# Optimization experiments

Hardware: AMD Instinct MI355X
Metric: run time of the kernel (lower is better)

Reference implementation:

```python
import jax, jax.numpy as jnp
import numpy as np

N_GRAPHS = 1024
N_NODES = 65536
N_EDGES = 262144
D = 256          # node/edge/global feature dim
D_IN = 3 * D     # concat of edge_agg, node_agg, globals
D_HID = 512
D_OUT = 256


def setup_inputs() -> dict:
    key = jax.random.key(0)
    ks = jax.random.split(key, 9)
    nodes = jax.random.normal(ks[0], (N_NODES, D), dtype=jnp.float32)
    edges = jax.random.normal(ks[1], (N_EDGES, D), dtype=jnp.float32)
    globals_ = jax.random.normal(ks[2], (N_GRAPHS, D), dtype=jnp.float32)
    node_graph_ids = jnp.sort(jax.random.randint(ks[3], (N_NODES,), 0, N_GRAPHS, dtype=jnp.int32))
    edge_graph_ids = jnp.sort(jax.random.randint(ks[4], (N_EDGES,), 0, N_GRAPHS, dtype=jnp.int32))
    W1 = jax.random.normal(ks[5], (D_IN, D_HID), dtype=jnp.float32) * (1.0 / np.sqrt(D_IN))
    b1 = jnp.zeros((D_HID,), dtype=jnp.float32)
    W2 = jax.random.normal(ks[6], (D_HID, D_OUT), dtype=jnp.float32) * (1.0 / np.sqrt(D_HID))
    b2 = jnp.zeros((D_OUT,), dtype=jnp.float32)
    return {"nodes": nodes, "edges": edges, "globals_": globals_,
            "node_graph_ids": node_graph_ids, "edge_graph_ids": edge_graph_ids,
            "W1": W1, "b1": b1, "W2": W2, "b2": b2}


def reference(nodes, edges, globals_, node_graph_ids, edge_graph_ids, W1, b1, W2, b2):
    G = globals_.shape[0]
    # EdgesToGlobalsAggregator / NodesToGlobalsAggregator: unsorted segment sum per graph
    edge_agg = jax.ops.segment_sum(edges, edge_graph_ids, num_segments=G)  # [G, D]
    node_agg = jax.ops.segment_sum(nodes, node_graph_ids, num_segments=G)  # [G, D]
    collected = jnp.concatenate([edge_agg, node_agg, globals_], axis=-1)   # [G, 3D]
    # global_model: 2-layer MLP with ReLU
    h = jax.nn.relu(collected @ W1 + b1)
    updated_globals = h @ W2 + b2
    return updated_globals
```

## Files before the change

kernel.cpp:

```cpp
#include <hip/hip_runtime.h>

#define G      1024
#define NNODES 65536
#define NEDGES 262144
#define D      256
#define DIN    768
#define DHID   512
#define DOUT   256

__device__ __forceinline__ int lower_bound(const int* __restrict__ a, int n, int key) {
    int lo = 0, hi = n;
    while (lo < hi) {
        const int mid = (lo + hi) >> 1;
        if (a[mid] < key) lo = mid + 1; else hi = mid;
    }
    return lo;
}

__global__ __launch_bounds__(256) void fused_agg(
        const float4* __restrict__ nodes,
        const float4* __restrict__ edges,
        const float4* __restrict__ globals_,
        const int* __restrict__ nids,
        const int* __restrict__ eids,
        float* __restrict__ collected) {
    const int g    = blockIdx.x;
    const int lane = threadIdx.x & 63;
    const int wave = threadIdx.x >> 6;

    const int es = lower_bound(eids, NEDGES, g);
    const int ee = lower_bound(eids, NEDGES, g + 1);
    const int ns = lower_bound(nids, NNODES, g);
    const int ne = lower_bound(nids, NNODES, g + 1);

    float4 acc_e = {0.f, 0.f, 0.f, 0.f};
    {
        int r = es + wave;
        for (; r + 28 < ee; r += 32) {
            const float4 v0 = edges[(size_t)(r +  0) * (D / 4) + lane];
            const float4 v1 = edges[(size_t)(r +  4) * (D / 4) + lane];
            const float4 v2 = edges[(size_t)(r +  8) * (D / 4) + lane];
            const float4 v3 = edges[(size_t)(r + 12) * (D / 4) + lane];
            const float4 v4 = edges[(size_t)(r + 16) * (D / 4) + lane];
            const float4 v5 = edges[(size_t)(r + 20) * (D / 4) + lane];
            const float4 v6 = edges[(size_t)(r + 24) * (D / 4) + lane];
            const float4 v7 = edges[(size_t)(r + 28) * (D / 4) + lane];
            acc_e.x += ((v0.x + v1.x) + (v2.x + v3.x)) + ((v4.x + v5.x) + (v6.x + v7.x));
            acc_e.y += ((v0.y + v1.y) + (v2.y + v3.y)) + ((v4.y + v5.y) + (v6.y + v7.y));
            acc_e.z += ((v0.z + v1.z) + (v2.z + v3.z)) + ((v4.z + v5.z) + (v6.z + v7.z));
            acc_e.w += ((v0.w + v1.w) + (v2.w + v3.w)) + ((v4.w + v5.w) + (v6.w + v7.w));
        }
        for (; r < ee; r += 4) {
            const float4 v = edges[(size_t)r * (D / 4) + lane];
            acc_e.x += v.x; acc_e.y += v.y; acc_e.z += v.z; acc_e.w += v.w;
        }
    }

    float4 acc_n = {0.f, 0.f, 0.f, 0.f};
    {
        int r = ns + wave;
        for (; r + 28 < ne; r += 32) {
            const float4 v0 = nodes[(size_t)(r +  0) * (D / 4) + lane];
            const float4 v1 = nodes[(size_t)(r +  4) * (D / 4) + lane];
            const float4 v2 = nodes[(size_t)(r +  8) * (D / 4) + lane];
            const float4 v3 = nodes[(size_t)(r + 12) * (D / 4) + lane];
            const float4 v4 = nodes[(size_t)(r + 16) * (D / 4) + lane];
            const float4 v5 = nodes[(size_t)(r + 20) * (D / 4) + lane];
            const float4 v6 = nodes[(size_t)(r + 24) * (D / 4) + lane];
            const float4 v7 = nodes[(size_t)(r + 28) * (D / 4) + lane];
            acc_n.x += ((v0.x + v1.x) + (v2.x + v3.x)) + ((v4.x + v5.x) + (v6.x + v7.x));
            acc_n.y += ((v0.y + v1.y) + (v2.y + v3.y)) + ((v4.y + v5.y) + (v6.y + v7.y));
            acc_n.z += ((v0.z + v1.z) + (v2.z + v3.z)) + ((v4.z + v5.z) + (v6.z + v7.z));
            acc_n.w += ((v0.w + v1.w) + (v2.w + v3.w)) + ((v4.w + v5.w) + (v6.w + v7.w));
        }
        for (; r < ne; r += 4) {
            const float4 v = nodes[(size_t)r * (D / 4) + lane];
            acc_n.x += v.x; acc_n.y += v.y; acc_n.z += v.z; acc_n.w += v.w;
        }
    }

    __shared__ __align__(16) float se[4][D];
    __shared__ __align__(16) float sn[4][D];
    *(float4*)&se[wave][lane * 4] = acc_e;
    *(float4*)&sn[wave][lane * 4] = acc_n;
    __syncthreads();

    const int t = threadIdx.x;
    const float ev = (se[0][t] + se[1][t]) + (se[2][t] + se[3][t]);
    const float nv = (sn[0][t] + sn[1][t]) + (sn[2][t] + sn[3][t]);
    float* row = collected + (size_t)g * DIN;
    row[t]         = ev;
    row[D + t]     = nv;
    row[2 * D + t] = ((const float*)globals_)[(size_t)g * D + t];
}

template <int TM, int TN, int TK>
__global__ __launch_bounds__(256) void gemm_bias_act(
        const float* __restrict__ A, const float* __restrict__ B,
        const float* __restrict__ bias, float* __restrict__ C,
        int M, int N, int K, int relu) {
    __shared__ float At[2][TK][TM + 2];
    __shared__ __align__(16) float Bs[2][TK][TN];

    const int tid = threadIdx.x;
    const int tx = tid & 15;
    const int ty = tid >> 4;
    const int m0 = blockIdx.y * TM;
    const int n0 = blockIdx.x * TN;

    const int ar = tid >> 3;
    const int ac = (tid & 7) * 4;
    const int br = tid >> 3;
    const int bc = (tid & 7) * 8;

    const float* Aptr = A + (size_t)(m0 + ar) * K + ac;
    const float* Bptr = B + (size_t)br * N + n0 + bc;

    {
        const float4 a4  = *(const float4*)Aptr;
        const float4 b40 = *(const float4*)Bptr;
        const float4 b41 = *(const float4*)(Bptr + 4);
        At[0][ac + 0][ar] = a4.x; At[0][ac + 1][ar] = a4.y;
        At[0][ac + 2][ar] = a4.z; At[0][ac + 3][ar] = a4.w;
        *(float4*)&Bs[0][br][bc]     = b40;
        *(float4*)&Bs[0][br][bc + 4] = b41;
    }
    __syncthreads();

    float4 acc0 = {0.f, 0.f, 0.f, 0.f};
    float4 acc1 = {0.f, 0.f, 0.f, 0.f};
    int buf = 0;

    for (int kt = 0; kt < K; kt += TK) {
        const bool has_next = (kt + TK) < K;
        float4 na, nb0, nb1;
        if (has_next) {
            na  = *(const float4*)(Aptr + kt + TK);
            nb0 = *(const float4*)(Bptr + (size_t)(kt + TK) * N);
            nb1 = *(const float4*)(Bptr + (size_t)(kt + TK) * N + 4);
        }
#pragma unroll
        for (int k = 0; k < TK; ++k) {
            const float2 a2 = *(const float2*)&At[buf][k][ty * 2];
            const float4 bv = *(const float4*)&Bs[buf][k][tx * 4];
            acc0.x += a2.x * bv.x; acc0.y += a2.x * bv.y;
            acc0.z += a2.x * bv.z; acc0.w += a2.x * bv.w;
            acc1.x += a2.y * bv.x; acc1.y += a2.y * bv.y;
            acc1.z += a2.y * bv.z; acc1.w += a2.y * bv.w;
        }
        if (has_next) {
            const int nb = buf ^ 1;
            At[nb][ac + 0][ar] = na.x; At[nb][ac + 1][ar] = na.y;
            At[nb][ac + 2][ar] = na.z; At[nb][ac + 3][ar] = na.w;
            *(float4*)&Bs[nb][br][bc]     = nb0;
            *(float4*)&Bs[nb][br][bc + 4] = nb1;
            __syncthreads();
            buf = nb;
        }
    }

    const int col = n0 + tx * 4;
    const int row = m0 + ty * 2;
    const float4 bv = *(const float4*)&bias[col];
    float4 o0, o1;
    o0.x = acc0.x + bv.x; o0.y = acc0.y + bv.y; o0.z = acc0.z + bv.z; o0.w = acc0.w + bv.w;
    o1.x = acc1.x + bv.x; o1.y = acc1.y + bv.y; o1.z = acc1.z + bv.z; o1.w = acc1.w + bv.w;
    if (relu) {
        o0.x = fmaxf(o0.x, 0.f); o0.y = fmaxf(o0.y, 0.f);
        o0.z = fmaxf(o0.z, 0.f); o0.w = fmaxf(o0.w, 0.f);
        o1.x = fmaxf(o1.x, 0.f); o1.y = fmaxf(o1.y, 0.f);
        o1.z = fmaxf(o1.z, 0.f); o1.w = fmaxf(o1.w, 0.f);
    }
    *(float4*)&C[(size_t)row * N + col] = o0;
    *(float4*)&C[(size_t)(row + 1) * N + col] = o1;
}

extern "C" void kernel_launch(void* const* d_in, const int* in_sizes, int n_in,
                              void* d_out, int out_size, void* d_ws, size_t ws_size,
                              hipStream_t stream) {
    const float* nodes    = (const float*)d_in[0];
    const float* edges    = (const float*)d_in[1];
    const float* globals_ = (const float*)d_in[2];
    const int*   nids     = (const int*)d_in[3];
    const int*   eids     = (const int*)d_in[4];
    const float* W1       = (const float*)d_in[5];
    const float* b1       = (const float*)d_in[6];
    const float* W2       = (const float*)d_in[7];
    const float* b2       = (const float*)d_in[8];
    float* out = (float*)d_out;

    float* collected = (float*)d_ws;
    float* h         = collected + (size_t)G * DIN;

    fused_agg<<<G, 256, 0, stream>>>(
        (const float4*)nodes, (const float4*)edges, (const float4*)globals_,
        nids, eids, collected);

    gemm_bias_act<32, 64, 32><<<dim3(DHID / 64, G / 32), 256, 0, stream>>>(
        collected, W1, b1, h, G, DHID, DIN, 1);

    gemm_bias_act<32, 64, 32><<<dim3(DOUT / 64, G / 32), 256, 0, stream>>>(
        h, W2, b2, out, G, DOUT, DHID, 0);
}
```

Measured before the change: 465.2 us.

## Fuse aggregation and both MLP GEMMs into one persistent kernel with group counters

Replaces three kernel launches with a single 512-block kernel. Each block aggregates two graphs, then computes GEMM1 tiles and GEMM2 tiles, waiting on per-row-group atomic counters instead of kernel boundaries. The aim is to remove launch gaps and tail idle time between stages, and to let GEMM work start as soon as its 32 input rows are ready. The cost is a memset launch for the counters and spin-waits that depend on all 512 blocks being resident at once (launch_bounds 256,2), which deadlocks if they are not co-resident.

```diff
diff --git a/kernel.cpp b/kernel.cpp
--- a/kernel.cpp
+++ b/kernel.cpp
@@ -8,6 +8,12 @@
 #define DHID   512
 #define DOUT   256
 
+#define NBLK   512
+#define GRP    32
+#define NGRP   (G / GRP)
+#define G1_BLOCKS (NGRP * (DHID / 64))
+#define G2_BLOCKS (NGRP * (DOUT / 64))
+
 __device__ __forceinline__ int lower_bound(const int* __restrict__ a, int n, int key) {
     int lo = 0, hi = n;
     while (lo < hi) {
@@ -17,14 +23,13 @@
     return lo;
 }
 
-__global__ __launch_bounds__(256) void fused_agg(
-        const float4* __restrict__ nodes,
-        const float4* __restrict__ edges,
-        const float4* __restrict__ globals_,
-        const int* __restrict__ nids,
-        const int* __restrict__ eids,
-        float* __restrict__ collected) {
-    const int g    = blockIdx.x;
+struct LdsRed { float se[4][D]; float sn[4][D]; };
+struct LdsGemm { float At[2][32][34]; float Bs[2][32][64]; };
+
+__device__ __forceinline__ void aggregate_one(
+        int g, const float4* __restrict__ nodes, const float4* __restrict__ edges,
+        const float4* __restrict__ globals_, const int* __restrict__ nids,
+        const int* __restrict__ eids, float* __restrict__ collected, LdsRed* red) {
     const int lane = threadIdx.x & 63;
     const int wave = threadIdx.x >> 6;
 
@@ -55,7 +60,6 @@
             acc_e.x += v.x; acc_e.y += v.y; acc_e.z += v.z; acc_e.w += v.w;
         }
     }
-
     float4 acc_n = {0.f, 0.f, 0.f, 0.f};
     {
         int r = ns + wave;
@@ -79,35 +83,27 @@
         }
     }
 
-    __shared__ __align__(16) float se[4][D];
-    __shared__ __align__(16) float sn[4][D];
-    *(float4*)&se[wave][lane * 4] = acc_e;
-    *(float4*)&sn[wave][lane * 4] = acc_n;
+    *(float4*)&red->se[wave][lane * 4] = acc_e;
+    *(float4*)&red->sn[wave][lane * 4] = acc_n;
     __syncthreads();
 
     const int t = threadIdx.x;
-    const float ev = (se[0][t] + se[1][t]) + (se[2][t] + se[3][t]);
-    const float nv = (sn[0][t] + sn[1][t]) + (sn[2][t] + sn[3][t]);
+    const float ev = (red->se[0][t] + red->se[1][t]) + (red->se[2][t] + red->se[3][t]);
+    const float nv = (red->sn[0][t] + red->sn[1][t]) + (red->sn[2][t] + red->sn[3][t]);
     float* row = collected + (size_t)g * DIN;
     row[t]         = ev;
     row[D + t]     = nv;
     row[2 * D + t] = ((const float*)globals_)[(size_t)g * D + t];
 }
 
-template <int TM, int TN, int TK>
-__global__ __launch_bounds__(256) void gemm_bias_act(
+__device__ __forceinline__ void gemm_tile(
         const float* __restrict__ A, const float* __restrict__ B,
         const float* __restrict__ bias, float* __restrict__ C,
-        int M, int N, int K, int relu) {
-    __shared__ float At[2][TK][TM + 2];
-    __shared__ __align__(16) float Bs[2][TK][TN];
-
+        const int N, const int K, const int relu, const int m0, const int n0,
+        LdsGemm* gg) {
     const int tid = threadIdx.x;
     const int tx = tid & 15;
     const int ty = tid >> 4;
-    const int m0 = blockIdx.y * TM;
-    const int n0 = blockIdx.x * TN;
-
     const int ar = tid >> 3;
     const int ac = (tid & 7) * 4;
     const int br = tid >> 3;
@@ -120,10 +116,10 @@
         const float4 a4  = *(const float4*)Aptr;
         const float4 b40 = *(const float4*)Bptr;
         const float4 b41 = *(const float4*)(Bptr + 4);
-        At[0][ac + 0][ar] = a4.x; At[0][ac + 1][ar] = a4.y;
-        At[0][ac + 2][ar] = a4.z; At[0][ac + 3][ar] = a4.w;
-        *(float4*)&Bs[0][br][bc]     = b40;
-        *(float4*)&Bs[0][br][bc + 4] = b41;
+        gg->At[0][ac + 0][ar] = a4.x; gg->At[0][ac + 1][ar] = a4.y;
+        gg->At[0][ac + 2][ar] = a4.z; gg->At[0][ac + 3][ar] = a4.w;
+        *(float4*)&gg->Bs[0][br][bc]     = b40;
+        *(float4*)&gg->Bs[0][br][bc + 4] = b41;
     }
     __syncthreads();
 
@@ -131,18 +127,18 @@
     float4 acc1 = {0.f, 0.f, 0.f, 0.f};
     int buf = 0;
 
-    for (int kt = 0; kt < K; kt += TK) {
-        const bool has_next = (kt + TK) < K;
+    for (int kt = 0; kt < K; kt += 32) {
+        const bool has_next = (kt + 32) < K;
         float4 na, nb0, nb1;
         if (has_next) {
-            na  = *(const float4*)(Aptr + kt + TK);
-            nb0 = *(const float4*)(Bptr + (size_t)(kt + TK) * N);
-            nb1 = *(const float4*)(Bptr + (size_t)(kt + TK) * N + 4);
+            na  = *(const float4*)(Aptr + kt + 32);
+            nb0 = *(const float4*)(Bptr + (size_t)(kt + 32) * N);
+            nb1 = *(const float4*)(Bptr + (size_t)(kt + 32) * N + 4);
         }
 #pragma unroll
-        for (int k = 0; k < TK; ++k) {
-            const float2 a2 = *(const float2*)&At[buf][k][ty * 2];
-            const float4 bv = *(const float4*)&Bs[buf][k][tx * 4];
+        for (int k = 0; k < 32; ++k) {
+            const float2 a2 = *(const float2*)&gg->At[buf][k][ty * 2];
+            const float4 bv = *(const float4*)&gg->Bs[buf][k][tx * 4];
             acc0.x += a2.x * bv.x; acc0.y += a2.x * bv.y;
             acc0.z += a2.x * bv.z; acc0.w += a2.x * bv.w;
             acc1.x += a2.y * bv.x; acc1.y += a2.y * bv.y;
@@ -150,10 +146,10 @@
         }
         if (has_next) {
             const int nb = buf ^ 1;
-            At[nb][ac + 0][ar] = na.x; At[nb][ac + 1][ar] = na.y;
-            At[nb][ac + 2][ar] = na.z; At[nb][ac + 3][ar] = na.w;
-            *(float4*)&Bs[nb][br][bc]     = nb0;
-            *(float4*)&Bs[nb][br][bc + 4] = nb1;
+            gg->At[nb][ac + 0][ar] = na.x; gg->At[nb][ac + 1][ar] = na.y;
+            gg->At[nb][ac + 2][ar] = na.z; gg->At[nb][ac + 3][ar] = na.w;
+            *(float4*)&gg->Bs[nb][br][bc]     = nb0;
+            *(float4*)&gg->Bs[nb][br][bc + 4] = nb1;
             __syncthreads();
             buf = nb;
         }
@@ -175,30 +171,82 @@
     *(float4*)&C[(size_t)(row + 1) * N + col] = o1;
 }
 
+__device__ __forceinline__ void signal_group(unsigned int* c) {
+    __threadfence();
+    __syncthreads();
+    if (threadIdx.x == 0)
+        __hip_atomic_fetch_add(c, 1u, __ATOMIC_RELEASE, __HIP_MEMORY_SCOPE_AGENT);
+}
+
+__device__ __forceinline__ void wait_group(unsigned int* c, unsigned int target) {
+    if (threadIdx.x == 0)
+        while (__hip_atomic_load(c, __ATOMIC_RELAXED, __HIP_MEMORY_SCOPE_AGENT) < target)
+            __builtin_amdgcn_s_sleep(2);
+    __syncthreads();
+    __builtin_amdgcn_fence(__ATOMIC_ACQUIRE, "agent");
+}
+
+__global__ __launch_bounds__(256, 2) void fused_all(
+        const float4* __restrict__ nodes,
+        const float4* __restrict__ edges,
+        const float4* __restrict__ globals_,
+        const int* __restrict__ nids,
+        const int* __restrict__ eids,
+        const float* __restrict__ W1, const float* __restrict__ b1,
+        const float* __restrict__ W2, const float* __restrict__ b2,
+        float* __restrict__ collected, float* __restrict__ h,
+        float* __restrict__ out,
+        unsigned int* __restrict__ cnt1, unsigned int* __restrict__ cnt2) {
+    __shared__ __align__(16) union { LdsRed red; LdsGemm gg; } lds;
+
+    const int b = blockIdx.x;
+
+    aggregate_one(b, nodes, edges, globals_, nids, eids, collected, &lds.red);
+    signal_group(&cnt1[b >> 5]);
+    __syncthreads();
+    aggregate_one(b + NBLK, nodes, edges, globals_, nids, eids, collected, &lds.red);
+    signal_group(&cnt1[(b + NBLK) >> 5]);
+
+    if (b >= G1_BLOCKS) return;
+
+    {
+        const int mg = b >> 3, ng = b & 7;
+        wait_group(&cnt1[mg], GRP);
+        gemm_tile(collected, W1, b1, h, DHID, DIN, 1, mg * 32, ng * 64, &lds.gg);
+    }
+    signal_group(&cnt2[b >> 3]);
+
+    if (b >= G2_BLOCKS) return;
+
+    {
+        const int mg = b >> 2, ng = b & 3;
+        wait_group(&cnt2[mg], 8u);
+        gemm_tile(h, W2, b2, out, DOUT, DHID, 0, mg * 32, ng * 64, &lds.gg);
+    }
+}
+
 extern "C" void kernel_launch(void* const* d_in, const int* in_sizes, int n_in,
                               void* d_out, int out_size, void* d_ws, size_t ws_size,
                               hipStream_t stream) {
-    const float* nodes    = (const float*)d_in[0];
-    const float* edges    = (const float*)d_in[1];
-    const float* globals_ = (const float*)d_in[2];
-    const int*   nids     = (const int*)d_in[3];
-    const int*   eids     = (const int*)d_in[4];
-    const float* W1       = (const float*)d_in[5];
-    const float* b1       = (const float*)d_in[6];
-    const float* W2       = (const float*)d_in[7];
-    const float* b2       = (const float*)d_in[8];
+    const float4* nodes    = (const float4*)d_in[0];
+    const float4* edges    = (const float4*)d_in[1];
+    const float4* globals_ = (const float4*)d_in[2];
+    const int*    nids     = (const int*)d_in[3];
+    const int*    eids     = (const int*)d_in[4];
+    const float*  W1       = (const float*)d_in[5];
+    const float*  b1       = (const float*)d_in[6];
+    const float*  W2       = (const float*)d_in[7];
+    const float*  b2       = (const float*)d_in[8];
     float* out = (float*)d_out;
 
     float* collected = (float*)d_ws;
     float* h         = collected + (size_t)G * DIN;
-
-    fused_agg<<<G, 256, 0, stream>>>(
-        (const float4*)nodes, (const float4*)edges, (const float4*)globals_,
-        nids, eids, collected);
-
-    gemm_bias_act<32, 64, 32><<<dim3(DHID / 64, G / 32), 256, 0, stream>>>(
-        collected, W1, b1, h, G, DHID, DIN, 1);
-
-    gemm_bias_act<32, 64, 32><<<dim3(DOUT / 64, G / 32), 256, 0, stream>>>(
-        h, W2, b2, out, G, DOUT, DHID, 0);
-}
+    unsigned int* cnt1 = (unsigned int*)((char*)d_ws + (size_t)(G * DIN + G * DHID) * sizeof(float));
+    unsigned int* cnt2 = cnt1 + NGRP;
+
+    hipMemsetAsync(cnt1, 0, 2 * NGRP * sizeof(unsigned int), stream);
+
+    fused_all<<<NBLK, 256, 0, stream>>>(
+        nodes, edges, globals_, nids, eids, W1, b1, W2, b2,
+        collected, h, out, cnt1, cnt2);
+}
```

New measurement: 679.1 us. 1.46x slower.

## Precompute segment offsets in a separate kernel and widen aggregation blocks to 8 waves

Applied to the files above, without the earlier changes.

Moves the four per-block binary searches into a small build_offsets kernel that writes CSR-style offset arrays to the workspace, so each aggregation block just reads two pairs of ints. The aggregation kernel now runs 512 threads (8 waves) per graph, each wave striding by 8 rows with an 8-deep unroll, which puts more loads in flight per segment. Final reduction is split so half the threads sum edges and half sum nodes. This costs an extra kernel launch, and with about 256 edge rows per graph the unrolled loop runs only a few iterations per wave, so more of the work falls into the remainder loop.

```diff
diff --git a/kernel.cpp b/kernel.cpp
--- a/kernel.cpp
+++ b/kernel.cpp
@@ -17,81 +17,94 @@
     return lo;
 }
 
-__global__ __launch_bounds__(256) void fused_agg(
+__global__ __launch_bounds__(256) void build_offsets(
+        const int* __restrict__ eids, const int* __restrict__ nids,
+        int* __restrict__ eoff, int* __restrict__ noff) {
+    const int t = blockIdx.x * 256 + threadIdx.x;
+    if (t <= G)              eoff[t]         = lower_bound(eids, NEDGES, t);
+    else if (t <= 2 * G + 1) noff[t - G - 1] = lower_bound(nids, NNODES, t - G - 1);
+}
+
+__global__ __launch_bounds__(512, 8) void fused_agg(
         const float4* __restrict__ nodes,
         const float4* __restrict__ edges,
         const float4* __restrict__ globals_,
-        const int* __restrict__ nids,
-        const int* __restrict__ eids,
+        const int* __restrict__ eoff,
+        const int* __restrict__ noff,
         float* __restrict__ collected) {
+    __shared__ __align__(16) float se[8][D];
+    __shared__ __align__(16) float sn[8][D];
+
     const int g    = blockIdx.x;
     const int lane = threadIdx.x & 63;
     const int wave = threadIdx.x >> 6;
 
-    const int es = lower_bound(eids, NEDGES, g);
-    const int ee = lower_bound(eids, NEDGES, g + 1);
-    const int ns = lower_bound(nids, NNODES, g);
-    const int ne = lower_bound(nids, NNODES, g + 1);
-
-    float4 acc_e = {0.f, 0.f, 0.f, 0.f};
+    const int es = eoff[g], ee = eoff[g + 1];
+    const int ns = noff[g], ne = noff[g + 1];
+
     {
+        float4 acc = {0.f, 0.f, 0.f, 0.f};
         int r = es + wave;
-        for (; r + 28 < ee; r += 32) {
-            const float4 v0 = edges[(size_t)(r +  0) * (D / 4) + lane];
-            const float4 v1 = edges[(size_t)(r +  4) * (D / 4) + lane];
-            const float4 v2 = edges[(size_t)(r +  8) * (D / 4) + lane];
-            const float4 v3 = edges[(size_t)(r + 12) * (D / 4) + lane];
-            const float4 v4 = edges[(size_t)(r + 16) * (D / 4) + lane];
-            const float4 v5 = edges[(size_t)(r + 20) * (D / 4) + lane];
-            const float4 v6 = edges[(size_t)(r + 24) * (D / 4) + lane];
-            const float4 v7 = edges[(size_t)(r + 28) * (D / 4) + lane];
-            acc_e.x += ((v0.x + v1.x) + (v2.x + v3.x)) + ((v4.x + v5.x) + (v6.x + v7.x));
-            acc_e.y += ((v0.y + v1.y) + (v2.y + v3.y)) + ((v4.y + v5.y) + (v6.y + v7.y));
-            acc_e.z += ((v0.z + v1.z) + (v2.z + v3.z)) + ((v4.z + v5.z) + (v6.z + v7.z));
-            acc_e.w += ((v0.w + v1.w) + (v2.w + v3.w)) + ((v4.w + v5.w) + (v6.w + v7.w));
-        }
-        for (; r < ee; r += 4) {
+        for (; r + 56 < ee; r += 64) {
+            const float4* p = edges + (size_t)r * (D / 4) + lane;
+            const float4 v0 = p[0 * 8 * (D / 4)];
+            const float4 v1 = p[1 * 8 * (D / 4)];
+            const float4 v2 = p[2 * 8 * (D / 4)];
+            const float4 v3 = p[3 * 8 * (D / 4)];
+            const float4 v4 = p[4 * 8 * (D / 4)];
+            const float4 v5 = p[5 * 8 * (D / 4)];
+            const float4 v6 = p[6 * 8 * (D / 4)];
+            const float4 v7 = p[7 * 8 * (D / 4)];
+            acc.x += ((v0.x + v1.x) + (v2.x + v3.x)) + ((v4.x + v5.x) + (v6.x + v7.x));
+            acc.y += ((v0.y + v1.y) + (v2.y + v3.y)) + ((v4.y + v5.y) + (v6.y + v7.y));
+            acc.z += ((v0.z + v1.z) + (v2.z + v3.z)) + ((v4.z + v5.z) + (v6.z + v7.z));
+            acc.w += ((v0.w + v1.w) + (v2.w + v3.w)) + ((v4.w + v5.w) + (v6.w + v7.w));
+        }
+        for (; r < ee; r += 8) {
             const float4 v = edges[(size_t)r * (D / 4) + lane];
-            acc_e.x += v.x; acc_e.y += v.y; acc_e.z += v.z; acc_e.w += v.w;
-        }
-    }
-
-    float4 acc_n = {0.f, 0.f, 0.f, 0.f};
+            acc.x += v.x; acc.y += v.y; acc.z += v.z; acc.w += v.w;
+        }
+        *(float4*)&se[wave][lane * 4] = acc;
+    }
     {
+        float4 acc = {0.f, 0.f, 0.f, 0.f};
         int r = ns + wave;
-        for (; r + 28 < ne; r += 32) {
-            const float4 v0 = nodes[(size_t)(r +  0) * (D / 4) + lane];
-            const float4 v1 = nodes[(size_t)(r +  4) * (D / 4) + lane];
-            const float4 v2 = nodes[(size_t)(r +  8) * (D / 4) + lane];
-            const float4 v3 = nodes[(size_t)(r + 12) * (D / 4) + lane];
-            const float4 v4 = nodes[(size_t)(r + 16) * (D / 4) + lane];
-            const float4 v5 = nodes[(size_t)(r + 20) * (D / 4) + lane];
-            const float4 v6 = nodes[(size_t)(r + 24) * (D / 4) + lane];
-            const float4 v7 = nodes[(size_t)(r + 28) * (D / 4) + lane];
-            acc_n.x += ((v0.x + v1.x) + (v2.x + v3.x)) + ((v4.x + v5.x) + (v6.x + v7.x));
-            acc_n.y += ((v0.y + v1.y) + (v2.y + v3.y)) + ((v4.y + v5.y) + (v6.y + v7.y));
-            acc_n.z += ((v0.z + v1.z) + (v2.z + v3.z)) + ((v4.z + v5.z) + (v6.z + v7.z));
-            acc_n.w += ((v0.w + v1.w) + (v2.w + v3.w)) + ((v4.w + v5.w) + (v6.w + v7.w));
-        }
-        for (; r < ne; r += 4) {
+        for (; r + 56 < ne; r += 64) {
+            const float4* p = nodes + (size_t)r * (D / 4) + lane;
+            const float4 v0 = p[0 * 8 * (D / 4)];
+            const float4 v1 = p[1 * 8 * (D / 4)];
+            const float4 v2 = p[2 * 8 * (D / 4)];
+            const float4 v3 = p[3 * 8 * (D / 4)];
+            const float4 v4 = p[4 * 8 * (D / 4)];
+            const float4 v5 = p[5 * 8 * (D / 4)];
+            const float4 v6 = p[6 * 8 * (D / 4)];
+            const float4 v7 = p[7 * 8 * (D / 4)];
+            acc.x += ((v0.x + v1.x) + (v2.x + v3.x)) + ((v4.x + v5.x) + (v6.x + v7.x));
+            acc.y += ((v0.y + v1.y) + (v2.y + v3.y)) + ((v4.y + v5.y) + (v6.y + v7.y));
+            acc.z += ((v0.z + v1.z) + (v2.z + v3.z)) + ((v4.z + v5.z) + (v6.z + v7.z));
+            acc.w += ((v0.w + v1.w) + (v2.w + v3.w)) + ((v4.w + v5.w) + (v6.w + v7.w));
+        }
+        for (; r < ne; r += 8) {
             const float4 v = nodes[(size_t)r * (D / 4) + lane];
-            acc_n.x += v.x; acc_n.y += v.y; acc_n.z += v.z; acc_n.w += v.w;
-        }
-    }
-
-    __shared__ __align__(16) float se[4][D];
-    __shared__ __align__(16) float sn[4][D];
-    *(float4*)&se[wave][lane * 4] = acc_e;
-    *(float4*)&sn[wave][lane * 4] = acc_n;
+            acc.x += v.x; acc.y += v.y; acc.z += v.z; acc.w += v.w;
+        }
+        *(float4*)&sn[wave][lane * 4] = acc;
+    }
     __syncthreads();
 
-    const int t = threadIdx.x;
-    const float ev = (se[0][t] + se[1][t]) + (se[2][t] + se[3][t]);
-    const float nv = (sn[0][t] + sn[1][t]) + (sn[2][t] + sn[3][t]);
     float* row = collected + (size_t)g * DIN;
-    row[t]         = ev;
-    row[D + t]     = nv;
-    row[2 * D + t] = ((const float*)globals_)[(size_t)g * D + t];
+    if (threadIdx.x < D) {
+        const int t = threadIdx.x;
+        const float ev = ((se[0][t] + se[1][t]) + (se[2][t] + se[3][t]))
+                       + ((se[4][t] + se[5][t]) + (se[6][t] + se[7][t]));
+        row[t]         = ev;
+        row[2 * D + t] = ((const float*)globals_)[(size_t)g * D + t];
+    } else {
+        const int t = threadIdx.x - D;
+        const float nv = ((sn[0][t] + sn[1][t]) + (sn[2][t] + sn[3][t]))
+                       + ((sn[4][t] + sn[5][t]) + (sn[6][t] + sn[7][t]));
+        row[D + t] = nv;
+    }
 }
 
 template <int TM, int TN, int TK>
@@ -191,10 +204,14 @@
 
     float* collected = (float*)d_ws;
     float* h         = collected + (size_t)G * DIN;
-
-    fused_agg<<<G, 256, 0, stream>>>(
+    int*   eoff      = (int*)(h + (size_t)G * DHID);
+    int*   noff      = eoff + (G + 1);
+
+    build_offsets<<<(2 * (G + 1) + 255) / 256, 256, 0, stream>>>(eids, nids, eoff, noff);
+
+    fused_agg<<<G, 512, 0, stream>>>(
         (const float4*)nodes, (const float4*)edges, (const float4*)globals_,
-        nids, eids, collected);
+        eoff, noff, collected);
 
     gemm_bias_act<32, 64, 32><<<dim3(DHID / 64, G / 32), 256, 0, stream>>>(
         collected, W1, b1, h, G, DHID, DIN, 1);
```

After: 464.0 us. Within noise of the previous version (-0.3%).

## Split segment sums into fixed row chunks with atomic flushes; read globals directly in GEMM

Applied to the files above, without the earlier changes.

Segment aggregation no longer runs one block per graph with binary-search bounds. Each wave now sums a fixed contiguous chunk of edge and node rows, tracking graph-id boundaries and flushing partial sums with atomicAdd into a zeroed buffer. This balances work across waves regardless of graph size and software-pipelines the loads. The first GEMM reads the globals input directly through a split-A loader instead of copying it into the concatenated buffer. The cost is an extra memset, float atomics that make summation order nondeterministic, and chunk sizes hardcoded to the exact row counts.

```diff
diff --git a/kernel.cpp b/kernel.cpp
--- a/kernel.cpp
+++ b/kernel.cpp
@@ -7,117 +7,122 @@
 #define DIN    768
 #define DHID   512
 #define DOUT   256
-
-__device__ __forceinline__ int lower_bound(const int* __restrict__ a, int n, int key) {
-    int lo = 0, hi = n;
-    while (lo < hi) {
-        const int mid = (lo + hi) >> 1;
-        if (a[mid] < key) lo = mid + 1; else hi = mid;
-    }
-    return lo;
-}
-
-__global__ __launch_bounds__(256) void fused_agg(
+#define CW     512
+
+#define AGG_BLOCKS 1024
+#define EROWS      64
+#define NROWS      16
+
+__device__ __forceinline__ void flush_acc(float* __restrict__ dst, int cur, int col,
+                                          float4& acc) {
+    float* p = dst + (size_t)cur * CW + col;
+    atomicAdd(p + 0, acc.x); atomicAdd(p + 1, acc.y);
+    atomicAdd(p + 2, acc.z); atomicAdd(p + 3, acc.w);
+    acc.x = acc.y = acc.z = acc.w = 0.f;
+}
+
+__device__ __forceinline__ void row_step(int id, const float4 v, int& cur, float4& acc,
+                                         float* __restrict__ dst, int col) {
+    if (id != cur) { flush_acc(dst, cur, col, acc); cur = id; }
+    acc.x += v.x; acc.y += v.y; acc.z += v.z; acc.w += v.w;
+}
+
+__device__ __forceinline__ void load_group(const float4* __restrict__ src,
+                                           const int* __restrict__ ids, int r, int lane,
+                                           float4 v[8], int4& i0, int4& i1) {
+    const float4* p = src + (size_t)r * (D / 4) + lane;
+#pragma unroll
+    for (int j = 0; j < 8; ++j) v[j] = p[j * (D / 4)];
+    i0 = *(const int4*)&ids[r];
+    i1 = *(const int4*)&ids[r + 4];
+}
+
+__device__ __forceinline__ void proc_group(const float4 v[8], int4 i0, int4 i1,
+                                           int& cur, float4& acc,
+                                           float* __restrict__ dst, int col) {
+    if (i0.x == cur && i1.w == cur) {
+        acc.x += ((v[0].x + v[1].x) + (v[2].x + v[3].x)) + ((v[4].x + v[5].x) + (v[6].x + v[7].x));
+        acc.y += ((v[0].y + v[1].y) + (v[2].y + v[3].y)) + ((v[4].y + v[5].y) + (v[6].y + v[7].y));
+        acc.z += ((v[0].z + v[1].z) + (v[2].z + v[3].z)) + ((v[4].z + v[5].z) + (v[6].z + v[7].z));
+        acc.w += ((v[0].w + v[1].w) + (v[2].w + v[3].w)) + ((v[4].w + v[5].w) + (v[6].w + v[7].w));
+    } else {
+        row_step(i0.x, v[0], cur, acc, dst, col);
+        row_step(i0.y, v[1], cur, acc, dst, col);
+        row_step(i0.z, v[2], cur, acc, dst, col);
+        row_step(i0.w, v[3], cur, acc, dst, col);
+        row_step(i1.x, v[4], cur, acc, dst, col);
+        row_step(i1.y, v[5], cur, acc, dst, col);
+        row_step(i1.z, v[6], cur, acc, dst, col);
+        row_step(i1.w, v[7], cur, acc, dst, col);
+    }
+}
+
+__device__ __forceinline__ void seg_sum_pipelined(
+        const float4* __restrict__ src, const int* __restrict__ ids,
+        float* __restrict__ dst, int col, int r, int ngroups, int lane) {
+    float4 va[8], vb[8];
+    int4 ia0, ia1, ib0, ib1;
+    float4 acc = {0.f, 0.f, 0.f, 0.f};
+    int cur = ids[r];
+
+    load_group(src, ids, r, lane, va, ia0, ia1);
+    for (int gpair = 0; gpair < ngroups / 2 - 1; ++gpair) {
+        load_group(src, ids, r + 8, lane, vb, ib0, ib1);
+        proc_group(va, ia0, ia1, cur, acc, dst, col);
+        r += 8;
+        load_group(src, ids, r + 8, lane, va, ia0, ia1);
+        proc_group(vb, ib0, ib1, cur, acc, dst, col);
+        r += 8;
+    }
+    load_group(src, ids, r + 8, lane, vb, ib0, ib1);
+    proc_group(va, ia0, ia1, cur, acc, dst, col);
+    proc_group(vb, ib0, ib1, cur, acc, dst, col);
+    flush_acc(dst, cur, col, acc);
+}
+
+__global__ __launch_bounds__(256, 4) void fused_agg(
         const float4* __restrict__ nodes,
         const float4* __restrict__ edges,
-        const float4* __restrict__ globals_,
         const int* __restrict__ nids,
         const int* __restrict__ eids,
         float* __restrict__ collected) {
-    const int g    = blockIdx.x;
     const int lane = threadIdx.x & 63;
     const int wave = threadIdx.x >> 6;
-
-    const int es = lower_bound(eids, NEDGES, g);
-    const int ee = lower_bound(eids, NEDGES, g + 1);
-    const int ns = lower_bound(nids, NNODES, g);
-    const int ne = lower_bound(nids, NNODES, g + 1);
-
-    float4 acc_e = {0.f, 0.f, 0.f, 0.f};
-    {
-        int r = es + wave;
-        for (; r + 28 < ee; r += 32) {
-            const float4 v0 = edges[(size_t)(r +  0) * (D / 4) + lane];
-            const float4 v1 = edges[(size_t)(r +  4) * (D / 4) + lane];
-            const float4 v2 = edges[(size_t)(r +  8) * (D / 4) + lane];
-            const float4 v3 = edges[(size_t)(r + 12) * (D / 4) + lane];
-            const float4 v4 = edges[(size_t)(r + 16) * (D / 4) + lane];
-            const float4 v5 = edges[(size_t)(r + 20) * (D / 4) + lane];
-            const float4 v6 = edges[(size_t)(r + 24) * (D / 4) + lane];
-            const float4 v7 = edges[(size_t)(r + 28) * (D / 4) + lane];
-            acc_e.x += ((v0.x + v1.x) + (v2.x + v3.x)) + ((v4.x + v5.x) + (v6.x + v7.x));
-            acc_e.y += ((v0.y + v1.y) + (v2.y + v3.y)) + ((v4.y + v5.y) + (v6.y + v7.y));
-            acc_e.z += ((v0.z + v1.z) + (v2.z + v3.z)) + ((v4.z + v5.z) + (v6.z + v7.z));
-            acc_e.w += ((v0.w + v1.w) + (v2.w + v3.w)) + ((v4.w + v5.w) + (v6.w + v7.w));
-        }
-        for (; r < ee; r += 4) {
-            const float4 v = edges[(size_t)r * (D / 4) + lane];
-            acc_e.x += v.x; acc_e.y += v.y; acc_e.z += v.z; acc_e.w += v.w;
-        }
-    }
-
-    float4 acc_n = {0.f, 0.f, 0.f, 0.f};
-    {
-        int r = ns + wave;
-        for (; r + 28 < ne; r += 32) {
-            const float4 v0 = nodes[(size_t)(r +  0) * (D / 4) + lane];
-            const float4 v1 = nodes[(size_t)(r +  4) * (D / 4) + lane];
-            const float4 v2 = nodes[(size_t)(r +  8) * (D / 4) + lane];
-            const float4 v3 = nodes[(size_t)(r + 12) * (D / 4) + lane];
-            const float4 v4 = nodes[(size_t)(r + 16) * (D / 4) + lane];
-            const float4 v5 = nodes[(size_t)(r + 20) * (D / 4) + lane];
-            const float4 v6 = nodes[(size_t)(r + 24) * (D / 4) + lane];
-            const float4 v7 = nodes[(size_t)(r + 28) * (D / 4) + lane];
-            acc_n.x += ((v0.x + v1.x) + (v2.x + v3.x)) + ((v4.x + v5.x) + (v6.x + v7.x));
-            acc_n.y += ((v0.y + v1.y) + (v2.y + v3.y)) + ((v4.y + v5.y) + (v6.y + v7.y));
-            acc_n.z += ((v0.z + v1.z) + (v2.z + v3.z)) + ((v4.z + v5.z) + (v6.z + v7.z));
-            acc_n.w += ((v0.w + v1.w) + (v2.w + v3.w)) + ((v4.w + v5.w) + (v6.w + v7.w));
-        }
-        for (; r < ne; r += 4) {
-            const float4 v = nodes[(size_t)r * (D / 4) + lane];
-            acc_n.x += v.x; acc_n.y += v.y; acc_n.z += v.z; acc_n.w += v.w;
-        }
-    }
-
-    __shared__ __align__(16) float se[4][D];
-    __shared__ __align__(16) float sn[4][D];
-    *(float4*)&se[wave][lane * 4] = acc_e;
-    *(float4*)&sn[wave][lane * 4] = acc_n;
-    __syncthreads();
-
-    const int t = threadIdx.x;
-    const float ev = (se[0][t] + se[1][t]) + (se[2][t] + se[3][t]);
-    const float nv = (sn[0][t] + sn[1][t]) + (sn[2][t] + sn[3][t]);
-    float* row = collected + (size_t)g * DIN;
-    row[t]         = ev;
-    row[D + t]     = nv;
-    row[2 * D + t] = ((const float*)globals_)[(size_t)g * D + t];
-}
-
-template <int TM, int TN, int TK>
+    const int W    = blockIdx.x * 4 + wave;
+
+    seg_sum_pipelined(edges, eids, collected, lane * 4,       W * EROWS, EROWS / 8, lane);
+    seg_sum_pipelined(nodes, nids, collected, D + lane * 4,   W * NROWS, NROWS / 8, lane);
+}
+
 __global__ __launch_bounds__(256) void gemm_bias_act(
-        const float* __restrict__ A, const float* __restrict__ B,
+        const float* __restrict__ A1, const float* __restrict__ A2,
+        const float* __restrict__ B,
         const float* __restrict__ bias, float* __restrict__ C,
-        int M, int N, int K, int relu) {
-    __shared__ float At[2][TK][TM + 2];
-    __shared__ __align__(16) float Bs[2][TK][TN];
+        int N, int K, int asplit, int s1, int s2, int relu) {
+    __shared__ float At[2][32][34];
+    __shared__ __align__(16) float Bs[2][32][64];
 
     const int tid = threadIdx.x;
     const int tx = tid & 15;
     const int ty = tid >> 4;
-    const int m0 = blockIdx.y * TM;
-    const int n0 = blockIdx.x * TN;
+    const int m0 = blockIdx.y * 32;
+    const int n0 = blockIdx.x * 64;
 
     const int ar = tid >> 3;
     const int ac = (tid & 7) * 4;
     const int br = tid >> 3;
     const int bc = (tid & 7) * 8;
 
-    const float* Aptr = A + (size_t)(m0 + ar) * K + ac;
+    const int arow = m0 + ar;
     const float* Bptr = B + (size_t)br * N + n0 + bc;
 
+    auto loadA = [&](int kc) -> float4 {
+        return (kc < asplit) ? *(const float4*)&A1[(size_t)arow * s1 + kc + ac]
+                             : *(const float4*)&A2[(size_t)arow * s2 + (kc - asplit) + ac];
+    };
+
     {
-        const float4 a4  = *(const float4*)Aptr;
+        const float4 a4  = loadA(0);
         const float4 b40 = *(const float4*)Bptr;
         const float4 b41 = *(const float4*)(Bptr + 4);
         At[0][ac + 0][ar] = a4.x; At[0][ac + 1][ar] = a4.y;
@@ -131,16 +136,16 @@
     float4 acc1 = {0.f, 0.f, 0.f, 0.f};
     int buf = 0;
 
-    for (int kt = 0; kt < K; kt += TK) {
-        const bool has_next = (kt + TK) < K;
+    for (int kt = 0; kt < K; kt += 32) {
+        const bool has_next = (kt + 32) < K;
         float4 na, nb0, nb1;
         if (has_next) {
-            na  = *(const float4*)(Aptr + kt + TK);
-            nb0 = *(const float4*)(Bptr + (size_t)(kt + TK) * N);
-            nb1 = *(const float4*)(Bptr + (size_t)(kt + TK) * N + 4);
+            na  = loadA(kt + 32);
+            nb0 = *(const float4*)(Bptr + (size_t)(kt + 32) * N);
+            nb1 = *(const float4*)(Bptr + (size_t)(kt + 32) * N + 4);
         }
 #pragma unroll
-        for (int k = 0; k < TK; ++k) {
+        for (int k = 0; k < 32; ++k) {
             const float2 a2 = *(const float2*)&At[buf][k][ty * 2];
             const float4 bv = *(const float4*)&Bs[buf][k][tx * 4];
             acc0.x += a2.x * bv.x; acc0.y += a2.x * bv.y;
@@ -190,15 +195,16 @@
     float* out = (float*)d_out;
 
     float* collected = (float*)d_ws;
-    float* h         = collected + (size_t)G * DIN;
-
-    fused_agg<<<G, 256, 0, stream>>>(
-        (const float4*)nodes, (const float4*)edges, (const float4*)globals_,
-        nids, eids, collected);
-
-    gemm_bias_act<32, 64, 32><<<dim3(DHID / 64, G / 32), 256, 0, stream>>>(
-        collected, W1, b1, h, G, DHID, DIN, 1);
-
-    gemm_bias_act<32, 64, 32><<<dim3(DOUT / 64, G / 32), 256, 0, stream>>>(
-        h, W2, b2, out, G, DOUT, DHID, 0);
-}
+    float* h         = collected + (size_t)G * CW;
+
+    hipMemsetAsync(collected, 0, (size_t)G * CW * sizeof(float), stream);
+
+    fused_agg<<<AGG_BLOCKS, 256, 0, stream>>>(
+        (const float4*)nodes, (const float4*)edges, nids, eids, collected);
+
+    gemm_bias_act<<<dim3(DHID / 64, G / 32), 256, 0, stream>>>(
+        collected, globals_, W1, b1, h, DHID, DIN, CW, CW, D, 1);
+
+    gemm_bias_act<<<dim3(DOUT / 64, G / 32), 256, 0, stream>>>(
+        h, h, W2, b2, out, DOUT, DHID, DHID, DHID, DHID, 0);
+}
```

Measured after the change: 456.0 us. -2.0%, faster.
